# Kernel tuning notes

Hardware: AMD Instinct MI355X
Metric: run time of the kernel (lower is better)

The kernel has to match this reference:

```python
import jax, jax.numpy as jnp
import numpy as np

B, TOPK, H, I, E = 128, 8, 2048, 1408, 16


def setup_inputs() -> dict:
    key = jax.random.key(0)
    ks = jax.random.split(key, 8)
    x = jax.random.normal(ks[0], (B, H), dtype=jnp.float32)
    expert_ids = jax.random.randint(ks[1], (B, TOPK), 0, E, dtype=jnp.int32)
    smooth_scales = jax.random.uniform(ks[2], (E, I), dtype=jnp.float32, minval=0.5, maxval=1.5)
    expert_scales = jax.random.uniform(ks[3], (B, TOPK), dtype=jnp.float32)
    expert_scales = expert_scales / jnp.sum(expert_scales, axis=-1, keepdims=True)
    x_active_mask = jnp.ones((B,), dtype=bool)
    # int8-valued quantized expert weights (stored int32 for portability)
    w1 = jax.random.randint(ks[4], (E, H, 2 * I), -127, 128, dtype=jnp.int32)
    w1_scale = jax.random.uniform(ks[5], (E, 2 * I), dtype=jnp.float32, minval=1e-3, maxval=1e-2)
    w2 = jax.random.randint(ks[6], (E, I, H), -127, 128, dtype=jnp.int32)
    w2_scale = jax.random.uniform(ks[7], (E, H), dtype=jnp.float32, minval=1e-3, maxval=1e-2)
    return {"x": x, "expert_ids": expert_ids, "smooth_scales": smooth_scales,
            "expert_scales": expert_scales, "x_active_mask": x_active_mask,
            "w1": w1, "w1_scale": w1_scale, "w2": w2, "w2_scale": w2_scale}


def reference(x, expert_ids, smooth_scales, expert_scales, x_active_mask,
              w1, w1_scale, w2, w2_scale):
    # --- dispatch: dynamic per-token int8 quantization of x ---
    sx = jnp.maximum(jnp.max(jnp.abs(x), axis=-1, keepdims=True), 1e-12) / 127.0  # [B,1]
    xq = jnp.round(jnp.clip(x / sx, -128.0, 127.0))  # int8 values, fp32 storage
    # --- grouped GEMM1 (dense-equivalent of per-expert grouped matmul) ---
    h = jnp.einsum('bh,ehf->bef', xq, w1.astype(jnp.float32))  # [B,E,2I] int32 accum
    h = h * sx[:, :, None] * w1_scale[None]  # dequant: x_scale * per-channel w_scale
    # --- SwiGLU activation ---
    gate, up = h[..., :I], h[..., I:]
    act = jax.nn.silu(gate) * up  # [B,E,I]
    # --- smooth + dynamic re-quantization for GEMM2 ---
    act = act * smooth_scales[None]  # [B,E,I]
    s2 = jnp.maximum(jnp.max(jnp.abs(act), axis=-1, keepdims=True), 1e-12) / 127.0  # [B,E,1]
    aq = jnp.round(jnp.clip(act / s2, -128.0, 127.0))
    # --- grouped GEMM2 + dequant ---
    o = jnp.einsum('bei,eih->beh', aq, w2.astype(jnp.float32))  # [B,E,H]
    o = o * s2 * w2_scale[None]
    # --- combine: weighted sum over routed experts (scatter expert_scales to one-hot) ---
    comb = jnp.zeros((x.shape[0], w1.shape[0]), dtype=x.dtype)
    comb = comb.at[jnp.arange(x.shape[0])[:, None], expert_ids].add(expert_scales)  # [B,E]
    y = jnp.einsum('beh,be->bh', o, comb)
    return y * x_active_mask[:, None].astype(y.dtype)
```

## Files before the change

kernel.cpp:

```cpp
#include <hip/hip_runtime.h>
#include <math.h>

#define NB 128
#define NTOPK 8
#define NH 2048
#define NI 1408
#define NE 16
#define NTWO_I 2816
#define RR 16
#define NCF 7
#define SLOTS_PER_E (NCF * RR)
#define MAXSLOTS (NE * SLOTS_PER_E)

#define LDS_REG 260

typedef int v4i __attribute__((ext_vector_type(4)));

__device__ __forceinline__ int pack4(int a, int b, int c, int d) {
    return (a & 0xff) | ((b & 0xff) << 8) | ((c & 0xff) << 16) | (d << 24);
}

__device__ __forceinline__ void gload_lds16(const int* g, int* l) {
    __builtin_amdgcn_global_load_lds(
        (const __attribute__((address_space(1))) void*)(const void*)g,
        (__attribute__((address_space(3))) void*)(void*)l, 16, 0, 0);
}

__global__ void k_quant_x(const float* __restrict__ x,
                          int* __restrict__ xq8d,
                          float* __restrict__ sxv) {
    int b = blockIdx.x;
    int t = threadIdx.x;
    const float* xr = x + (size_t)b * NH;
    float m = 0.0f;
    for (int j = t; j < NH; j += 256) m = fmaxf(m, fabsf(xr[j]));
    __shared__ float red[256];
    red[t] = m;
    __syncthreads();
    for (int s = 128; s > 0; s >>= 1) {
        if (t < s) red[t] = fmaxf(red[t], red[t + s]);
        __syncthreads();
    }
    float scale = fmaxf(red[0], 1e-12f) / 127.0f;
    if (t == 0) sxv[b] = scale;
    for (int g = t; g < NH / 4; g += 256) {
        int q[4];
#pragma unroll
        for (int u = 0; u < 4; ++u)
            q[u] = (int)rintf(fminf(fmaxf(xr[4 * g + u] / scale, -128.0f), 127.0f));
        xq8d[(size_t)b * (NH / 4) + g] = pack4(q[0], q[1], q[2], q[3]);
    }
}

__global__ void k_route(const int* __restrict__ expert_ids,
                        const float* __restrict__ expert_scales,
                        int* __restrict__ slot_b,
                        float* __restrict__ slot_w,
                        int* __restrict__ nce_arr) {
    __shared__ int cnt[NE];
    __shared__ int fill[NE];
    int t = threadIdx.x;
    if (t < NE) { cnt[t] = 0; fill[t] = 0; }
    __syncthreads();
    for (int p = t; p < NB * NTOPK; p += 256) atomicAdd(&cnt[expert_ids[p]], 1);
    __syncthreads();
    if (t < NE) {
        int c = (cnt[t] + RR - 1) / RR;
        nce_arr[t] = c < NCF ? c : NCF;
    }
    for (int s = t; s < MAXSLOTS; s += 256) {
        slot_b[s] = 0;
        slot_w[s] = 0.0f;
    }
    __syncthreads();
    for (int p = t; p < NB * NTOPK; p += 256) {
        int e = expert_ids[p];
        int pos = atomicAdd(&fill[e], 1);
        if (pos < SLOTS_PER_E) {
            slot_b[e * SLOTS_PER_E + pos] = p >> 3;
            slot_w[e * SLOTS_PER_E + pos] = expert_scales[p];
        }
    }
}

__global__ __launch_bounds__(256) void k_gemm1(
    const int* __restrict__ xq8d,
    const int* __restrict__ slot_b, const int* __restrict__ nce_arr,
    const int* __restrict__ w1, int* __restrict__ h) {
    __shared__ int smw[16 * LDS_REG];
    int e = blockIdx.y;
    int nce = nce_arr[e];
    if (nce == 0) return;
    int t = threadIdx.x;
    int wave = t >> 6;
    int lane = t & 63;
    int lm = lane & 15;
    int kl = lane >> 4;
    int slot0 = e * SLOTS_PER_E;
    int colb0 = blockIdx.x * 64;
    int colb = colb0 + wave * 16;

    int rb[NCF];
#pragma unroll
    for (int q = 0; q < NCF; ++q)
        rb[q] = (q < nce) ? slot_b[slot0 + q * RR + lm] : 0;

    const int* gq = w1 + (size_t)e * NH * NTWO_I
                    + (size_t)(wave * 16 + kl) * NTWO_I + colb0 + lm * 4;

    v4i acc[NCF];
#pragma unroll
    for (int q = 0; q < NCF; ++q) acc[q] = (v4i){0, 0, 0, 0};

    for (int kb = 0; kb < NH / 64; ++kb) {
#pragma unroll
        for (int i = 0; i < 4; ++i)
            gload_lds16(gq + (size_t)(i * 4) * NTWO_I,
                        smw + (wave * 4 + i) * LDS_REG);
        v4i av[NCF];
#pragma unroll
        for (int q = 0; q < NCF; ++q)
            if (q < nce)
                av[q] = *(const v4i*)(xq8d + (size_t)rb[q] * (NH / 4)
                                      + kb * 16 + kl * 4);
        __syncthreads();

        int wv[16];
#pragma unroll
        for (int j = 0; j < 16; ++j)
            wv[j] = smw[(kl * 4 + (j >> 2)) * LDS_REG + (j & 3) * 64
                        + wave * 16 + lm];
        v4i b = {pack4(wv[0], wv[1], wv[2], wv[3]),
                 pack4(wv[4], wv[5], wv[6], wv[7]),
                 pack4(wv[8], wv[9], wv[10], wv[11]),
                 pack4(wv[12], wv[13], wv[14], wv[15])};
#pragma unroll
        for (int q = 0; q < NCF; ++q)
            if (q < nce)
                acc[q] = __builtin_amdgcn_mfma_i32_16x16x64_i8(av[q], b, acc[q],
                                                               0, 0, 0);
        __syncthreads();
        gq += (size_t)64 * NTWO_I;
    }

#pragma unroll
    for (int q = 0; q < NCF; ++q) {
        if (q < nce) {
            int* hp = h + (size_t)(slot0 + q * RR) * NTWO_I + colb + lm;
#pragma unroll
            for (int r = 0; r < 4; ++r)
                hp[(size_t)(kl * 4 + r) * NTWO_I] = acc[q][r];
        }
    }
}

__global__ void k_act(const int* __restrict__ h, const float* __restrict__ sxv,
                      const int* __restrict__ slot_b, const int* __restrict__ nce_arr,
                      const float* __restrict__ w1_scale, const float* __restrict__ smooth,
                      int* __restrict__ aq8d, float* __restrict__ s2f) {
    int slot = blockIdx.x;
    int e = slot / SLOTS_PER_E;
    int within = slot - e * SLOTS_PER_E;
    if ((within >> 4) >= nce_arr[e]) return;
    int t = threadIdx.x;
    float sx = sxv[slot_b[slot]];
    const int* hr = h + (size_t)slot * NTWO_I;
    const float* w1s = w1_scale + (size_t)e * NTWO_I;
    const float* sm = smooth + (size_t)e * NI;

    float av[8];
    float m = 0.0f;
    int it = 0;
    for (int g = t; g < NI / 4; g += 256, ++it) {
#pragma unroll
        for (int u = 0; u < 4; ++u) {
            int j = 4 * g + u;
            float gt = (float)hr[j] * sx * w1s[j];
            float up = (float)hr[j + NI] * sx * w1s[j + NI];
            float a = (gt / (1.0f + expf(-gt))) * up * sm[j];
            av[it * 4 + u] = a;
            m = fmaxf(m, fabsf(a));
        }
    }
    __shared__ float red[256];
    red[t] = m;
    __syncthreads();
    for (int s = 128; s > 0; s >>= 1) {
        if (t < s) red[t] = fmaxf(red[t], red[t + s]);
        __syncthreads();
    }
    float s2 = fmaxf(red[0], 1e-12f) / 127.0f;
    if (t == 0) s2f[slot] = s2;
    it = 0;
    for (int g = t; g < NI / 4; g += 256, ++it) {
        int q[4];
#pragma unroll
        for (int u = 0; u < 4; ++u)
            q[u] = (int)rintf(fminf(fmaxf(av[it * 4 + u] / s2, -128.0f), 127.0f));
        aq8d[(size_t)slot * (NI / 4) + g] = pack4(q[0], q[1], q[2], q[3]);
    }
}

__global__ __launch_bounds__(256) void k_gemm2(
    const int* __restrict__ aq8d, const float* __restrict__ s2f,
    const int* __restrict__ slot_b, const float* __restrict__ slot_w,
    const int* __restrict__ nce_arr,
    const int* __restrict__ w2, const float* __restrict__ w2_scale,
    float* __restrict__ y) {
    __shared__ int smw[16 * LDS_REG];
    int e = blockIdx.y;
    int nce = nce_arr[e];
    if (nce == 0) return;
    int t = threadIdx.x;
    int wave = t >> 6;
    int lane = t & 63;
    int lm = lane & 15;
    int kl = lane >> 4;
    int slot0 = e * SLOTS_PER_E;
    int colb0 = blockIdx.x * 64;
    int colb = colb0 + wave * 16;

    const int* gq = w2 + (size_t)e * NI * NH
                    + (size_t)(wave * 16 + kl) * NH + colb0 + lm * 4;

    v4i acc[NCF];
#pragma unroll
    for (int q = 0; q < NCF; ++q) acc[q] = (v4i){0, 0, 0, 0};

    for (int kb = 0; kb < NI / 64; ++kb) {
#pragma unroll
        for (int i = 0; i < 4; ++i)
            gload_lds16(gq + (size_t)(i * 4) * NH,
                        smw + (wave * 4 + i) * LDS_REG);
        v4i av[NCF];
#pragma unroll
        for (int q = 0; q < NCF; ++q)
            if (q < nce)
                av[q] = *(const v4i*)(aq8d + (size_t)(slot0 + q * RR + lm) * (NI / 4)
                                      + kb * 16 + kl * 4);
        __syncthreads();

        int wv[16];
#pragma unroll
        for (int j = 0; j < 16; ++j)
            wv[j] = smw[(kl * 4 + (j >> 2)) * LDS_REG + (j & 3) * 64
                        + wave * 16 + lm];
        v4i b = {pack4(wv[0], wv[1], wv[2], wv[3]),
                 pack4(wv[4], wv[5], wv[6], wv[7]),
                 pack4(wv[8], wv[9], wv[10], wv[11]),
                 pack4(wv[12], wv[13], wv[14], wv[15])};
#pragma unroll
        for (int q = 0; q < NCF; ++q)
            if (q < nce)
                acc[q] = __builtin_amdgcn_mfma_i32_16x16x64_i8(av[q], b, acc[q],
                                                               0, 0, 0);
        __syncthreads();
        gq += (size_t)64 * NH;
    }

    float w2s = w2_scale[(size_t)e * NH + colb + lm];
#pragma unroll
    for (int q = 0; q < NCF; ++q) {
        if (q < nce) {
#pragma unroll
            for (int r = 0; r < 4; ++r) {
                int s = slot0 + q * RR + kl * 4 + r;
                float cf = s2f[s] * slot_w[s];
                if (cf != 0.0f)
                    atomicAdd(y + (size_t)slot_b[s] * NH + colb + lm,
                              (float)acc[q][r] * cf * w2s);
            }
        }
    }
}

extern "C" void kernel_launch(void* const* d_in, const int* in_sizes, int n_in,
                              void* d_out, int out_size, void* d_ws, size_t ws_size,
                              hipStream_t stream) {
    const float* x = (const float*)d_in[0];
    const int* expert_ids = (const int*)d_in[1];
    const float* smooth = (const float*)d_in[2];
    const float* expert_scales = (const float*)d_in[3];
    const int* w1 = (const int*)d_in[5];
    const float* w1_scale = (const float*)d_in[6];
    const int* w2 = (const int*)d_in[7];
    const float* w2_scale = (const float*)d_in[8];
    float* y = (float*)d_out;

    char* p = (char*)d_ws;
    int* xq8d = (int*)p;               p += (size_t)NB * (NH / 4) * 4;
    float* sxv = (float*)p;            p += NB * 4;
    int* slot_b = (int*)p;             p += MAXSLOTS * 4;
    float* slot_w = (float*)p;         p += MAXSLOTS * 4;
    int* nce_arr = (int*)p;            p += NE * 4;
    float* s2f = (float*)p;            p += MAXSLOTS * 4;
    int* h = (int*)p;                  p += (size_t)MAXSLOTS * NTWO_I * 4;
    int* aq8d = (int*)p;               p += (size_t)MAXSLOTS * (NI / 4) * 4;

    hipMemsetAsync(d_out, 0, (size_t)out_size * sizeof(float), stream);

    k_quant_x<<<NB, 256, 0, stream>>>(x, xq8d, sxv);
    k_route<<<1, 256, 0, stream>>>(expert_ids, expert_scales, slot_b, slot_w, nce_arr);
    dim3 g1(NTWO_I / 64, NE);
    k_gemm1<<<g1, 256, 0, stream>>>(xq8d, slot_b, nce_arr, w1, h);
    k_act<<<MAXSLOTS, 256, 0, stream>>>(h, sxv, slot_b, nce_arr, w1_scale, smooth,
                                        aq8d, s2f);
    dim3 g2(NH / 64, NE);
    k_gemm2<<<g2, 256, 0, stream>>>(aq8d, s2f, slot_b, slot_w, nce_arr,
                                    w2, w2_scale, y);
}
```

Before: 659.4 us.

## Double-buffer LDS weight tiles in both grouped GEMMs and vectorize act loads

Both grouped GEMM kernels now use two LDS buffers. The global-to-LDS load for the next K block is issued before the current block is read and run through MFMA, which also cuts the barriers per K step from two to one. The aim is to hide global load latency behind compute in what looks like a latency-bound weight stream. LDS use per block doubles, which may lower occupancy. The activation kernel also reads the gate and up rows as 128-bit vectors instead of scalar loads.

```diff
diff --git a/kernel.cpp b/kernel.cpp
--- a/kernel.cpp
+++ b/kernel.cpp
@@ -87,7 +87,7 @@
     const int* __restrict__ xq8d,
     const int* __restrict__ slot_b, const int* __restrict__ nce_arr,
     const int* __restrict__ w1, int* __restrict__ h) {
-    __shared__ int smw[16 * LDS_REG];
+    __shared__ int smw[2][16 * LDS_REG];
     int e = blockIdx.y;
     int nce = nce_arr[e];
     if (nce == 0) return;
@@ -112,36 +112,49 @@
 #pragma unroll
     for (int q = 0; q < NCF; ++q) acc[q] = (v4i){0, 0, 0, 0};
 
-    for (int kb = 0; kb < NH / 64; ++kb) {
-#pragma unroll
-        for (int i = 0; i < 4; ++i)
-            gload_lds16(gq + (size_t)(i * 4) * NTWO_I,
-                        smw + (wave * 4 + i) * LDS_REG);
-        v4i av[NCF];
-#pragma unroll
-        for (int q = 0; q < NCF; ++q)
-            if (q < nce)
-                av[q] = *(const v4i*)(xq8d + (size_t)rb[q] * (NH / 4)
-                                      + kb * 16 + kl * 4);
-        __syncthreads();
-
-        int wv[16];
-#pragma unroll
-        for (int j = 0; j < 16; ++j)
-            wv[j] = smw[(kl * 4 + (j >> 2)) * LDS_REG + (j & 3) * 64
-                        + wave * 16 + lm];
-        v4i b = {pack4(wv[0], wv[1], wv[2], wv[3]),
-                 pack4(wv[4], wv[5], wv[6], wv[7]),
-                 pack4(wv[8], wv[9], wv[10], wv[11]),
-                 pack4(wv[12], wv[13], wv[14], wv[15])};
-#pragma unroll
-        for (int q = 0; q < NCF; ++q)
-            if (q < nce)
-                acc[q] = __builtin_amdgcn_mfma_i32_16x16x64_i8(av[q], b, acc[q],
-                                                               0, 0, 0);
-        __syncthreads();
-        gq += (size_t)64 * NTWO_I;
-    }
+#define PH1(BUF, KB, SCOND, SBUF, SKB)                                          \
+    do {                                                                        \
+        v4i av[NCF];                                                            \
+        _Pragma("unroll")                                                       \
+        for (int q = 0; q < NCF; ++q)                                           \
+            if (q < nce)                                                        \
+                av[q] = *(const v4i*)(xq8d + (size_t)rb[q] * (NH / 4)           \
+                                      + (KB) * 16 + kl * 4);                    \
+        if (SCOND) {                                                            \
+            const int* gs = gq + (size_t)(SKB) * 64 * NTWO_I;                   \
+            _Pragma("unroll")                                                   \
+            for (int i = 0; i < 4; ++i)                                         \
+                gload_lds16(gs + (size_t)(i * 4) * NTWO_I,                      \
+                            &smw[SBUF][(wave * 4 + i) * LDS_REG]);              \
+        }                                                                       \
+        int wv[16];                                                             \
+        _Pragma("unroll")                                                       \
+        for (int j = 0; j < 16; ++j)                                            \
+            wv[j] = smw[BUF][(kl * 4 + (j >> 2)) * LDS_REG + (j & 3) * 64       \
+                             + wave * 16 + lm];                                 \
+        v4i bf = {pack4(wv[0], wv[1], wv[2], wv[3]),                            \
+                  pack4(wv[4], wv[5], wv[6], wv[7]),                            \
+                  pack4(wv[8], wv[9], wv[10], wv[11]),                          \
+                  pack4(wv[12], wv[13], wv[14], wv[15])};                       \
+        _Pragma("unroll")                                                       \
+        for (int q = 0; q < NCF; ++q)                                           \
+            if (q < nce)                                                        \
+                acc[q] = __builtin_amdgcn_mfma_i32_16x16x64_i8(av[q], bf,       \
+                                                               acc[q], 0, 0, 0);\
+        __syncthreads();                                                        \
+    } while (0)
+
+#pragma unroll
+    for (int i = 0; i < 4; ++i)
+        gload_lds16(gq + (size_t)(i * 4) * NTWO_I,
+                    &smw[0][(wave * 4 + i) * LDS_REG]);
+    __syncthreads();
+
+    for (int kb = 0; kb < NH / 64; kb += 2) {
+        PH1(0, kb, true, 1, kb + 1);
+        PH1(1, kb + 1, (kb + 2 < NH / 64), 0, kb + 2);
+    }
+#undef PH1
 
 #pragma unroll
     for (int q = 0; q < NCF; ++q) {
@@ -172,11 +185,13 @@
     float m = 0.0f;
     int it = 0;
     for (int g = t; g < NI / 4; g += 256, ++it) {
+        v4i gv = *(const v4i*)(hr + 4 * g);
+        v4i uv = *(const v4i*)(hr + NI + 4 * g);
 #pragma unroll
         for (int u = 0; u < 4; ++u) {
             int j = 4 * g + u;
-            float gt = (float)hr[j] * sx * w1s[j];
-            float up = (float)hr[j + NI] * sx * w1s[j + NI];
+            float gt = (float)gv[u] * sx * w1s[j];
+            float up = (float)uv[u] * sx * w1s[j + NI];
             float a = (gt / (1.0f + expf(-gt))) * up * sm[j];
             av[it * 4 + u] = a;
             m = fmaxf(m, fabsf(a));
@@ -207,7 +222,7 @@
     const int* __restrict__ nce_arr,
     const int* __restrict__ w2, const float* __restrict__ w2_scale,
     float* __restrict__ y) {
-    __shared__ int smw[16 * LDS_REG];
+    __shared__ int smw[2][16 * LDS_REG];
     int e = blockIdx.y;
     int nce = nce_arr[e];
     if (nce == 0) return;
@@ -227,36 +242,50 @@
 #pragma unroll
     for (int q = 0; q < NCF; ++q) acc[q] = (v4i){0, 0, 0, 0};
 
-    for (int kb = 0; kb < NI / 64; ++kb) {
-#pragma unroll
-        for (int i = 0; i < 4; ++i)
-            gload_lds16(gq + (size_t)(i * 4) * NH,
-                        smw + (wave * 4 + i) * LDS_REG);
-        v4i av[NCF];
-#pragma unroll
-        for (int q = 0; q < NCF; ++q)
-            if (q < nce)
-                av[q] = *(const v4i*)(aq8d + (size_t)(slot0 + q * RR + lm) * (NI / 4)
-                                      + kb * 16 + kl * 4);
-        __syncthreads();
-
-        int wv[16];
-#pragma unroll
-        for (int j = 0; j < 16; ++j)
-            wv[j] = smw[(kl * 4 + (j >> 2)) * LDS_REG + (j & 3) * 64
-                        + wave * 16 + lm];
-        v4i b = {pack4(wv[0], wv[1], wv[2], wv[3]),
-                 pack4(wv[4], wv[5], wv[6], wv[7]),
-                 pack4(wv[8], wv[9], wv[10], wv[11]),
-                 pack4(wv[12], wv[13], wv[14], wv[15])};
-#pragma unroll
-        for (int q = 0; q < NCF; ++q)
-            if (q < nce)
-                acc[q] = __builtin_amdgcn_mfma_i32_16x16x64_i8(av[q], b, acc[q],
-                                                               0, 0, 0);
-        __syncthreads();
-        gq += (size_t)64 * NH;
-    }
+#define PH2(BUF, KB, SCOND, SBUF, SKB)                                          \
+    do {                                                                        \
+        v4i av[NCF];                                                            \
+        _Pragma("unroll")                                                       \
+        for (int q = 0; q < NCF; ++q)                                           \
+            if (q < nce)                                                        \
+                av[q] = *(const v4i*)(aq8d                                      \
+                         + (size_t)(slot0 + q * RR + lm) * (NI / 4)             \
+                         + (KB) * 16 + kl * 4);                                 \
+        if (SCOND) {                                                            \
+            const int* gs = gq + (size_t)(SKB) * 64 * NH;                       \
+            _Pragma("unroll")                                                   \
+            for (int i = 0; i < 4; ++i)                                         \
+                gload_lds16(gs + (size_t)(i * 4) * NH,                          \
+                            &smw[SBUF][(wave * 4 + i) * LDS_REG]);              \
+        }                                                                       \
+        int wv[16];                                                             \
+        _Pragma("unroll")                                                       \
+        for (int j = 0; j < 16; ++j)                                            \
+            wv[j] = smw[BUF][(kl * 4 + (j >> 2)) * LDS_REG + (j & 3) * 64       \
+                             + wave * 16 + lm];                                 \
+        v4i bf = {pack4(wv[0], wv[1], wv[2], wv[3]),                            \
+                  pack4(wv[4], wv[5], wv[6], wv[7]),                            \
+                  pack4(wv[8], wv[9], wv[10], wv[11]),                          \
+                  pack4(wv[12], wv[13], wv[14], wv[15])};                       \
+        _Pragma("unroll")                                                       \
+        for (int q = 0; q < NCF; ++q)                                           \
+            if (q < nce)                                                        \
+                acc[q] = __builtin_amdgcn_mfma_i32_16x16x64_i8(av[q], bf,       \
+                                                               acc[q], 0, 0, 0);\
+        __syncthreads();                                                        \
+    } while (0)
+
+#pragma unroll
+    for (int i = 0; i < 4; ++i)
+        gload_lds16(gq + (size_t)(i * 4) * NH,
+                    &smw[0][(wave * 4 + i) * LDS_REG]);
+    __syncthreads();
+
+    for (int kb = 0; kb < NI / 64; kb += 2) {
+        PH2(0, kb, true, 1, kb + 1);
+        PH2(1, kb + 1, (kb + 2 < NI / 64), 0, kb + 2);
+    }
+#undef PH2
 
     float w2s = w2_scale[(size_t)e * NH + colb + lm];
 #pragma unroll
```

Measured after the change: 665.3 us. No clear change (+0.9%).
